# Kernel tuning notes

Measured on AMD Instinct MI355X. Metric: run time of the kernel, lower is better.

## Reference

```python
import jax, jax.numpy as jnp
import numpy as np

N = 50000      # nodes
E = 200000     # directed edges (before self loops)
F_IN = 78      # atom feature dim
H = 4          # heads
G = 512        # graphs in batch
HID = 1024
OUT = 128
NEG_SLOPE = 0.2


def gat_conv(x, edge_index, W, att_src, att_dst, bias, num_nodes):
    """PyG GATConv (concat=True, add_self_loops=True), eval mode (no dropout)."""
    heads, ch = att_src.shape
    h = (x @ W).reshape(num_nodes, heads, ch)          # [N,H,C]
    # add self loops
    loop = jnp.arange(num_nodes, dtype=edge_index.dtype)
    row = jnp.concatenate([edge_index[0], loop])        # source j
    col = jnp.concatenate([edge_index[1], loop])        # target i
    a_src = jnp.einsum('nhc,hc->nh', h, att_src)        # [N,H]
    a_dst = jnp.einsum('nhc,hc->nh', h, att_dst)
    e = jax.nn.leaky_relu(a_src[row] + a_dst[col], NEG_SLOPE)   # [Etot,H]
    # segment softmax over incoming edges of each target node
    m = jax.ops.segment_max(e, col, num_segments=num_nodes)
    e = jnp.exp(e - m[col])
    denom = jax.ops.segment_sum(e, col, num_segments=num_nodes)
    alpha = e / (denom[col] + 1e-16)                    # [Etot,H]
    msg = h[row] * alpha[:, :, None]                    # [Etot,H,C]
    out = jax.ops.segment_sum(msg, col, num_segments=num_nodes)
    return out.reshape(num_nodes, heads * ch) + bias


def setup_inputs() -> dict:
    key = jax.random.key(0)
    ks = jax.random.split(key, 20)
    def glorot(k, shape):
        fan = shape[0] + shape[-1]
        return jax.random.normal(k, shape, jnp.float32) * np.sqrt(2.0 / fan)
    x = jax.random.normal(ks[0], (N, F_IN), jnp.float32)
    edge_index = jax.random.randint(ks[1], (2, E), 0, N, jnp.int64)
    batch = jnp.sort(jax.random.randint(ks[2], (N,), 0, G, jnp.int64))
    d1 = F_IN
    d2 = F_IN * H
    d3 = F_IN * H * H
    return {
        'x': x, 'edge_index': edge_index, 'batch': batch,
        'W1': glorot(ks[3], (d1, H * d1)), 'as1': glorot(ks[4], (H, d1)),
        'ad1': glorot(ks[5], (H, d1)), 'b1': jnp.zeros((H * d1,), jnp.float32),
        'W2': glorot(ks[6], (d2, H * d2)), 'as2': glorot(ks[7], (H, d2)),
        'ad2': glorot(ks[8], (H, d2)), 'b2': jnp.zeros((H * d2,), jnp.float32),
        'W3': glorot(ks[9], (d3, d3)), 'as3': glorot(ks[10], (1, d3)),
        'ad3': glorot(ks[11], (1, d3)), 'b3': jnp.zeros((d3,), jnp.float32),
        'fc1_w': glorot(ks[12], (d3, HID)), 'fc1_b': jnp.zeros((HID,), jnp.float32),
        'fc2_w': glorot(ks[13], (HID, OUT)), 'fc2_b': jnp.zeros((OUT,), jnp.float32),
    }


def reference(x, edge_index, batch, W1, as1, ad1, b1, W2, as2, ad2, b2,
              W3, as3, ad3, b3, fc1_w, fc1_b, fc2_w, fc2_b):
    h = jax.nn.relu(gat_conv(x, edge_index, W1, as1, ad1, b1, N))
    h = jax.nn.relu(gat_conv(h, edge_index, W2, as2, ad2, b2, N))
    h = jax.nn.relu(gat_conv(h, edge_index, W3, as3, ad3, b3, N))
    g = jax.ops.segment_max(h, batch, num_segments=G)   # global max pool [G, 1248]
    g = jax.nn.relu(g @ fc1_w + fc1_b)
    # dropout is identity in eval mode
    out = jax.nn.relu(g @ fc2_w + fc2_b)
    return out
```

## Files before the change

kernel.cpp:

```cpp
#include <hip/hip_runtime.h>

using u16 = unsigned short;
using u32 = unsigned int;

typedef short s16x8 __attribute__((ext_vector_type(8)));
typedef float f32x4 __attribute__((ext_vector_type(4)));

static __device__ __forceinline__ float b2f(u16 u){ u32 x = ((u32)u) << 16; float f; __builtin_memcpy(&f, &x, 4); return f; }
static __device__ __forceinline__ u16 f2bf(float f){ u32 x; __builtin_memcpy(&x, &f, 4); x += 0x7fffu + ((x >> 16) & 1u); return (u16)(x >> 16); }

static __device__ __forceinline__ void async16(const u16* g, u16* l){
  __builtin_amdgcn_global_load_lds((const __attribute__((address_space(1))) u32*)g,
                                   (__attribute__((address_space(3))) u32*)l, 16, 0, 0);
}

__global__ void detect_flags(const u16* x, const int* ei, int* flags){
  if (blockIdx.x || threadIdx.x) return;
  int cf = 0;
  for (int i = 0; i < 128; ++i){
    int ex = (x[2*i] >> 7) & 0xff;
    if (ex >= 110 && ex <= 140) cf++;
  }
  flags[0] = (cf > 64) ? 1 : 0;
  int cz = 0;
  for (int i = 0; i < 128; ++i){ if (ei[2*i+1] != 0) cz++; }
  flags[1] = (cz > 64) ? 1 : 0;
}

__global__ void zero_u32(u32* p, int n){
  int i = blockIdx.x*256 + threadIdx.x;
  if (i < n) p[i] = 0;
}

__global__ void pad_copy_x(const void* xin, u16* xp, int Nreal, long tot, int F, int Fp, const int* flags){
  long idx = (long)blockIdx.x*256 + threadIdx.x;
  if (idx >= tot) return;
  int n = (int)(idx / Fp), f = (int)(idx - (long)n*Fp);
  u16 v = 0;
  if (n < Nreal && f < F){
    if (flags[0]) v = ((const u16*)xin)[(long)n*F + f];
    else          v = f2bf(((const float*)xin)[(long)n*F + f]);
  }
  xp[idx] = v;
}

__global__ void transpose_pad(const void* W, u16* Wt, int K, int Nsub, int Kp, int Np,
                              int ldW, int colOff, const int* flags){
  __shared__ u16 tile[32][33];
  int f0 = flags[0];
  int kb = blockIdx.x*32, nb = blockIdx.y*32;
  int tx = threadIdx.x & 31, ty = threadIdx.x >> 5;
  for (int dy = 0; dy < 32; dy += 8){
    int k = kb + dy + ty, n = nb + tx;
    u16 v = 0;
    if (k < K && n < Nsub){
      long src = (long)k*ldW + colOff + n;
      if (f0) v = ((const u16*)W)[src];
      else    v = f2bf(((const float*)W)[src]);
    }
    tile[dy+ty][tx] = v;
  }
  __syncthreads();
  for (int dy = 0; dy < 32; dy += 8){
    int n = nb + dy + ty, k = kb + tx;
    if (n < Np && k < Kp) Wt[(long)n*Kp + k] = tile[tx][dy+ty];
  }
}

__global__ void copy_vec5(const void* s0, u16* d0, int n0,
                          const void* s1, u16* d1, int n1,
                          const void* s2, u16* d2, int n2,
                          const void* s3, u16* d3, int n3,
                          const void* s4, u16* d4, int n4,
                          const int* flags){
  int i = blockIdx.x*256 + threadIdx.x;
  int f0 = flags[0];
  auto cv = [&](const void* s, int j)->u16{
    return f0 ? ((const u16*)s)[j] : f2bf(((const float*)s)[j]);
  };
  if (i < n0){ d0[i] = cv(s0, i); return; } i -= n0;
  if (i < n1){ d1[i] = cv(s1, i); return; } i -= n1;
  if (i < n2){ d2[i] = cv(s2, i); return; } i -= n2;
  if (i < n3){ d3[i] = cv(s3, i); return; } i -= n3;
  if (i < n4){ d4[i] = cv(s4, i); }
}

__global__ void copy_int3(const int* ei, const int* bat,
                          int* rowC, int* colC, int* bat32,
                          int E, int N, const int* flags){
  int i = blockIdx.x*256 + threadIdx.x;
  int f1 = flags[1];
  if (i < E){ rowC[i] = f1 ? ei[i] : ei[2*i]; return; } i -= E;
  if (i < E){ colC[i] = f1 ? ei[E + i] : ei[2*(E + i)]; return; } i -= E;
  if (i < N){ bat32[i] = f1 ? bat[i] : bat[2*i]; }
}

__global__ void hist_kernel(const int* __restrict__ colC, u32* cnt, int E){
  int e = blockIdx.x*256 + threadIdx.x;
  if (e < E) atomicAdd(&cnt[colC[e]], 1u);
}

__global__ void scan_local(const u32* __restrict__ cnt, u32* __restrict__ rowptr,
                           u32* __restrict__ bsum, int N){
  int blk = blockIdx.x, t = threadIdx.x;
  int i = blk*1024 + t;
  u32 v = (i < N) ? (cnt[i] + 1u) : 0u;
  u32 x = v;
  for (int off = 1; off < 64; off <<= 1){
    u32 y = __shfl_up(x, off);
    if ((t & 63) >= off) x += y;
  }
  __shared__ u32 ws[16];
  if ((t & 63) == 63) ws[t >> 6] = x;
  __syncthreads();
  if (t < 16){
    u32 y = ws[t];
    for (int off = 1; off < 16; off <<= 1){
      u32 z = __shfl_up(y, off);
      if (t >= off) y += z;
    }
    ws[t] = y;
  }
  __syncthreads();
  u32 base = (t >> 6) ? ws[(t >> 6) - 1] : 0u;
  u32 inc = base + x;
  if (i < N) rowptr[i + 1] = inc;
  if (t == 1023) bsum[blk] = inc;
}

__global__ void scan_bsums(const u32* __restrict__ bsum, u32* __restrict__ boff, int nb){
  int t = threadIdx.x;
  u32 v = (t < nb) ? bsum[t] : 0u;
  u32 x = v;
  for (int off = 1; off < 64; off <<= 1){
    u32 y = __shfl_up(x, off);
    if ((t & 63) >= off) x += y;
  }
  __shared__ u32 ws[16];
  if ((t & 63) == 63) ws[t >> 6] = x;
  __syncthreads();
  if (t < 16){
    u32 y = ws[t];
    for (int off = 1; off < 16; off <<= 1){
      u32 z = __shfl_up(y, off);
      if (t >= off) y += z;
    }
    ws[t] = y;
  }
  __syncthreads();
  u32 base = (t >> 6) ? ws[(t >> 6) - 1] : 0u;
  u32 inc = base + x;
  if (t < nb) boff[t] = inc - v;
}

__global__ void scan_fixup(u32* rowptr, const u32* __restrict__ boff, int N){
  int i = blockIdx.x*1024 + threadIdx.x;
  if (i < N) rowptr[i+1] += boff[blockIdx.x];
  if (i == 0) rowptr[0] = 0;
}

__global__ void fill_self(const u32* rowptr, int* eidx, u32* cursor, int N){
  int i = blockIdx.x*256 + threadIdx.x;
  if (i >= N) return;
  eidx[rowptr[i]] = i;
  cursor[i] = rowptr[i] + 1;
}

__global__ void fill_edges(const int* __restrict__ rowC, const int* __restrict__ colC,
                           u32* cursor, int* eidx, int E){
  int e = blockIdx.x*256 + threadIdx.x;
  if (e >= E) return;
  u32 pos = atomicAdd(&cursor[colC[e]], 1u);
  eidx[pos] = rowC[e];
}

__global__ void wproj(const void* W, const void* as, const void* ad,
                      float* wsrc, float* wdst, int Cin, int Cpad, int Chead, int ldW,
                      int H, const int* flags){
  int wid = blockIdx.x*4 + (threadIdx.x >> 6);
  if (wid >= H*Cpad) return;
  int h = wid / Cpad, c = wid - h*Cpad;
  int lane = threadIdx.x & 63;
  float s = 0.f, d = 0.f;
  if (c < Cin){
    int f0 = flags[0];
    long base = (long)c*ldW + (long)h*Chead;
    const long av0 = (long)h*Chead;
    for (int o = lane; o < Chead; o += 64){
      float wv = f0 ? b2f(((const u16*)W)[base+o]) : ((const float*)W)[base+o];
      float avv = f0 ? b2f(((const u16*)as)[av0+o]) : ((const float*)as)[av0+o];
      float dvv = f0 ? b2f(((const u16*)ad)[av0+o]) : ((const float*)ad)[av0+o];
      s += wv*avv; d += wv*dvv;
    }
    for (int off = 32; off; off >>= 1){ s += __shfl_down(s, off); d += __shfl_down(d, off); }
  }
  if (lane == 0){ wsrc[(long)h*Cpad+c] = s; wdst[(long)h*Cpad+c] = d; }
}

template<int H>
__global__ void attn_dots_v(const u16* __restrict__ xin, long ldx,
                            const float* __restrict__ wsrc, const float* __restrict__ wdst,
                            float* __restrict__ a_src, float* __restrict__ a_dst,
                            int Nn, int C){
  int node = blockIdx.x*4 + (threadIdx.x >> 6);
  if (node >= Nn) return;
  int lane = threadIdx.x & 63;
  const u16* xr = xin + (long)node*ldx;
  float s[H], d[H];
#pragma unroll
  for (int h = 0; h < H; ++h){ s[h] = 0.f; d[h] = 0.f; }
  for (int c = lane*8; c < C; c += 512){
    s16x8 xv = *(const s16x8*)&xr[c];
    float xf[8];
#pragma unroll
    for (int j = 0; j < 8; ++j) xf[j] = b2f((u16)xv[j]);
#pragma unroll
    for (int h = 0; h < H; ++h){
      f32x4 w0 = *(const f32x4*)&wsrc[h*C + c];
      f32x4 w1 = *(const f32x4*)&wsrc[h*C + c + 4];
      f32x4 d0 = *(const f32x4*)&wdst[h*C + c];
      f32x4 d1 = *(const f32x4*)&wdst[h*C + c + 4];
#pragma unroll
      for (int j = 0; j < 4; ++j){
        s[h] += xf[j]*w0[j] + xf[j+4]*w1[j];
        d[h] += xf[j]*d0[j] + xf[j+4]*d1[j];
      }
    }
  }
#pragma unroll
  for (int h = 0; h < H; ++h)
    for (int off = 32; off; off >>= 1){ s[h] += __shfl_down(s[h], off); d[h] += __shfl_down(d[h], off); }
  if (lane == 0){
#pragma unroll
    for (int h = 0; h < H; ++h){ a_src[(long)node*H+h] = s[h]; a_dst[(long)node*H+h] = d[h]; }
  }
}

__global__ void attn_stats(const u32* __restrict__ rowptr, const int* __restrict__ eidx,
                           const float* __restrict__ a_src, const float* __restrict__ a_dst,
                           u16* __restrict__ pbuf, float* __restrict__ invd, int NH, int H){
  int idx = blockIdx.x*256 + threadIdx.x;
  if (idx >= NH) return;
  int i = idx / H, hd = idx - i*H;
  u32 s0 = rowptr[i], s1 = rowptr[i+1];
  float ad = a_dst[idx];
  float m = -1e30f;
  for (u32 p = s0; p < s1; ++p){
    float e = a_src[eidx[p]*H + hd] + ad;
    e = e > 0.f ? e : 0.2f*e;
    m = fmaxf(m, e);
  }
  float den = 0.f;
  for (u32 p = s0; p < s1; ++p){
    float e = a_src[eidx[p]*H + hd] + ad;
    e = e > 0.f ? e : 0.2f*e;
    float v = __expf(e - m);
    pbuf[(long)p*H + hd] = f2bf(v);
    den += v;
  }
  invd[idx] = 1.f / (den + 1e-16f);
}

__global__ void aggregate_v(const u32* __restrict__ rowptr, const int* __restrict__ eidx,
                            const u16* __restrict__ pbuf, const float* __restrict__ invd,
                            const u16* __restrict__ xin, long ldx,
                            u16* __restrict__ xagg, long ldagg,
                            int chunks, int H, int headStride){
  int i = blockIdx.x;
  int t = threadIdx.x;
  if (t >= H*chunks) return;
  int h = t / chunks, ck = t - h*chunks;
  int c0 = ck*8;
  u32 s0 = rowptr[i], s1 = rowptr[i+1];
  float acc[8];
#pragma unroll
  for (int j = 0; j < 8; ++j) acc[j] = 0.f;
  u32 p = s0;
  for (; p + 2 <= s1; p += 2){
    int sa = eidx[p], sb = eidx[p+1];
    float wa = b2f(pbuf[(long)p*H + h]);
    float wb = b2f(pbuf[(long)(p+1)*H + h]);
    s16x8 va = *(const s16x8*)&xin[(long)sa*ldx + c0];
    s16x8 vb = *(const s16x8*)&xin[(long)sb*ldx + c0];
#pragma unroll
    for (int j = 0; j < 8; ++j) acc[j] += wa*b2f((u16)va[j]) + wb*b2f((u16)vb[j]);
  }
  if (p < s1){
    int sa = eidx[p];
    float wa = b2f(pbuf[(long)p*H + h]);
    s16x8 va = *(const s16x8*)&xin[(long)sa*ldx + c0];
#pragma unroll
    for (int j = 0; j < 8; ++j) acc[j] += wa*b2f((u16)va[j]);
  }
  float inv = invd[(long)i*H + h];
  s16x8 ov;
#pragma unroll
  for (int j = 0; j < 8; ++j) ov[j] = (short)f2bf(acc[j]*inv);
  *(s16x8*)&xagg[(long)i*ldagg + h*headStride + c0] = ov;
}

__global__ void pack_pool(const u32* __restrict__ poolf, u16* __restrict__ pooled, int n){
  int i = blockIdx.x*256 + threadIdx.x;
  if (i >= n) return;
  u32 b = poolf[i]; float f; __builtin_memcpy(&f, &b, 4);
  pooled[i] = f2bf(f);
}

template<int NH>
__global__ __launch_bounds__(256) void gemm_bt(
    const u16* __restrict__ Ag, long lda, const u16* __restrict__ Bg,
    const u16* __restrict__ bias, u16* __restrict__ Cg,
    int M, int Nstore, int K, long ldc, int mode, const int* flags,
    const int* __restrict__ batg, u32* poolf, long ldp,
    int nt, int mt, long hA, long hB, long hC)
{
  const int xcd = blockIdx.x & 7;
  const int g = blockIdx.x >> 3;
  const u16 *A, *B, *bi; u16* C;
  int ntile, m;
  if constexpr (NH > 1){
    const int nhnt = NH * nt;
    const int inner = g % nhnt;
    ntile = inner % nt;
    const int head = inner / nt;
    m = (g / nhnt)*8 + xcd;
    A = Ag + (long)head*hA; B = Bg + (long)head*hB;
    bi = bias + (long)head*hC; C = Cg + (long)head*hC;
  } else {
    ntile = g % nt;
    m = (g / nt)*8 + xcd;
    A = Ag; B = Bg; bi = bias; C = Cg;
  }
  if (m >= mt) return;

  __shared__ __align__(16) u16 As[128*32];
  __shared__ __align__(16) u16 Bs[128*32];
  const int tid = threadIdx.x;
  const int wave = tid >> 6, lane = tid & 63;
  const int quad = lane >> 4, mrow = lane & 15;
  const int wm = (wave >> 1) * 64, wn = (wave & 1) * 64;
  const long bm = (long)m * 128;
  const long bn = (long)ntile * 128;

  f32x4 acc[4][4];
#pragma unroll
  for (int i = 0; i < 4; i++)
#pragma unroll
    for (int j = 0; j < 4; j++) acc[i][j] = (f32x4){0.f, 0.f, 0.f, 0.f};

  const int r0 = wave*32 + (lane >> 2);
  const int r1 = r0 + 16;
  const int kcl = lane & 3;
  const int q0 = kcl ^ ((r0 >> 1) & 3);
  const int q1 = kcl ^ ((r1 >> 1) & 3);
  const u16* a0 = A + (bm + r0)*lda + q0*8;
  const u16* a1 = A + (bm + r1)*lda + q1*8;
  const u16* b0 = B + (bn + r0)*(long)K + q0*8;
  const u16* b1 = B + (bn + r1)*(long)K + q1*8;
  u16* la0 = &As[r0*32 + kcl*8];
  u16* la1 = &As[r1*32 + kcl*8];
  u16* lb0 = &Bs[r0*32 + kcl*8];
  u16* lb1 = &Bs[r1*32 + kcl*8];

  for (int k0 = 0; k0 < K; k0 += 32){
    async16(a0 + k0, la0);
    async16(a1 + k0, la1);
    async16(b0 + k0, lb0);
    async16(b1 + k0, lb1);
    __syncthreads();
    s16x8 af[4], bf[4];
#pragma unroll
    for (int i = 0; i < 4; i++){
      int r = wm + i*16 + mrow;
      int q = quad ^ ((r >> 1) & 3);
      af[i] = *(const s16x8*)&As[r*32 + q*8];
    }
#pragma unroll
    for (int j = 0; j < 4; j++){
      int r = wn + j*16 + mrow;
      int q = quad ^ ((r >> 1) & 3);
      bf[j] = *(const s16x8*)&Bs[r*32 + q*8];
    }
#pragma unroll
    for (int i = 0; i < 4; i++)
#pragma unroll
      for (int j = 0; j < 4; j++)
        acc[i][j] = __builtin_amdgcn_mfma_f32_16x16x32_bf16(af[i], bf[j], acc[i][j], 0, 0, 0);
    __syncthreads();
  }

  if (mode & 4){
    int garr[16];
#pragma unroll
    for (int i = 0; i < 4; i++)
#pragma unroll
      for (int r = 0; r < 4; r++){
        long row = bm + wm + i*16 + quad*4 + r;
        garr[i*4+r] = (row < M) ? batg[row] : -1;
      }
#pragma unroll
    for (int j = 0; j < 4; j++){
      long col = bn + wn + j*16 + mrow;
      if (col >= Nstore) continue;
      float bv = b2f(bi[col]);
      int curg = -1; float curm = 0.f;
#pragma unroll
      for (int i = 0; i < 4; i++)
#pragma unroll
        for (int r = 0; r < 4; r++){
          int g2 = garr[i*4+r];
          if (g2 >= 0){
            float v = fmaxf(acc[i][j][r] + bv, 0.f);
            if (g2 != curg){
              if (curg >= 0){
                u32 bits; __builtin_memcpy(&bits, &curm, 4);
                atomicMax(&poolf[(long)curg*ldp + col], bits);
              }
              curg = g2; curm = v;
            } else curm = fmaxf(curm, v);
          }
        }
      if (curg >= 0){
        u32 bits; __builtin_memcpy(&bits, &curm, 4);
        atomicMax(&poolf[(long)curg*ldp + col], bits);
      }
    }
    return;
  }

  const int f0 = (mode & 2) ? flags[0] : 1;
#pragma unroll
  for (int i = 0; i < 4; i++){
    long row0 = bm + wm + i*16 + quad*4;
#pragma unroll
    for (int j = 0; j < 4; j++){
      long col = bn + wn + j*16 + mrow;
      if (col < Nstore){
        float bv = (mode & 1) ? b2f(bi[col]) : 0.f;
#pragma unroll
        for (int r = 0; r < 4; r++){
          long row = row0 + r;
          if (row < M){
            float v = acc[i][j][r];
            if (mode & 1) v = fmaxf(v + bv, 0.f);
            if (f0) C[row*ldc + col] = f2bf(v);
            else    ((float*)C)[row*ldc + col] = v;
          }
        }
      }
    }
  }
}

extern "C" void kernel_launch(void* const* d_in, const int* in_sizes, int n_in,
                              void* d_out, int out_size, void* d_ws, size_t ws_size,
                              hipStream_t stream){
  const u16* x    = (const u16*)d_in[0];
  const int* ei   = (const int*)d_in[1];
  const int* bat  = (const int*)d_in[2];
  const void* W1  = d_in[3];
  const void* as1 = d_in[4]; const void* ad1 = d_in[5]; const void* b1 = d_in[6];
  const void* W2  = d_in[7];
  const void* as2 = d_in[8]; const void* ad2 = d_in[9]; const void* b2 = d_in[10];
  const void* W3  = d_in[11];
  const void* as3 = d_in[12]; const void* ad3 = d_in[13]; const void* b3 = d_in[14];
  const void* fc1w = d_in[15]; const void* fc1b = d_in[16];
  const void* fc2w = d_in[17]; const void* fc2b = d_in[18];

  const int E = in_sizes[1] / 2;
  const int N = in_sizes[2];
  const int G = 512, H = 4;
  const int Mpad = ((N + 127)/128)*128;
  const int Etot = E + N;
  const int Mt = Mpad/128;
  const int nb1024 = (N + 1023)/1024;
  const int Mg8 = ((Mt + 7)/8);

  char* w = (char*)d_ws;
  size_t off = 0;
  auto AL = [&](size_t b)->char*{ char* p = w + off; off = (off + b + 255) & ~(size_t)255; return p; };

  u16* P = (u16*)AL((size_t)Mpad*1248*2 + 512);
  u16* Q = (u16*)AL((size_t)Mpad*1248*2 + 512);
  u16* wt1 = (u16*)AL((size_t)4*128*96*2);
  u16* wt2 = (u16*)AL((size_t)4*384*320*2);
  u16* wt3 = (u16*)AL((size_t)1280*1248*2);
  u16* wf1 = (u16*)AL((size_t)1024*1248*2);
  u16* wf2 = (u16*)AL((size_t)128*1024*2);
  u16* cb1 = (u16*)AL(312*2);  u16* cb2 = (u16*)AL(1248*2); u16* cb3 = (u16*)AL(1248*2);
  u16* cbf1 = (u16*)AL(1024*2); u16* cbf2 = (u16*)AL(128*2);
  float* ws1 = (float*)AL(4*80*4);   float* wd1 = (float*)AL(4*80*4);
  float* ws2 = (float*)AL(4*312*4);  float* wd2 = (float*)AL(4*312*4);
  float* ws3 = (float*)AL(1248*4);   float* wd3 = (float*)AL(1248*4);
  float* a_src = (float*)AL((size_t)N*H*4);
  float* a_dst = (float*)AL((size_t)N*H*4);
  float* invd  = (float*)AL((size_t)N*H*4);
  u16*  pbuf   = (u16*)AL((size_t)Etot*H*2);
  u32* cnt     = (u32*)AL((size_t)N*4);
  u32* rowptr  = (u32*)AL((size_t)(N+1)*4);
  u32* bsum    = (u32*)AL((size_t)1024*4);
  u32* boff    = (u32*)AL((size_t)1024*4);
  int* eidx    = (int*)AL((size_t)Etot*4);
  int* bat32   = (int*)AL((size_t)N*4);
  u32* poolf   = (u32*)AL((size_t)G*1248*4);
  u16* pooled  = (u16*)AL((size_t)G*1248*2 + 512);
  u16* fc1o    = (u16*)AL((size_t)G*1024*2 + 512);
  int* flags   = (int*)AL(16);

  if (ws_size < off || n_in < 19) return;

  u16* xpad = (u16*)((char*)P + ((size_t)40 << 20));
  int* rowC = (int*)((char*)Q + ((size_t)64 << 20));
  int* colC = rowC + E;

  detect_flags<<<1, 64, 0, stream>>>(x, ei, flags);
  zero_u32<<<(N+255)/256, 256, 0, stream>>>(cnt, N);
  zero_u32<<<(G*1248+255)/256, 256, 0, stream>>>(poolf, G*1248);
  {
    long tot = (long)Mpad*96;
    pad_copy_x<<<(unsigned)((tot+255)/256), 256, 0, stream>>>(x, xpad, N, tot, 78, 96, flags);
  }
  for (int h = 0; h < 4; ++h)
    transpose_pad<<<dim3(3,4),  256, 0, stream>>>(W1, wt1 + h*128*96, 78, 78, 96, 128, 312, h*78, flags);
  for (int h = 0; h < 4; ++h)
    transpose_pad<<<dim3(10,12), 256, 0, stream>>>(W2, wt2 + h*384*320, 312, 312, 320, 384, 1248, h*312, flags);
  transpose_pad<<<dim3(39,40), 256, 0, stream>>>(W3,   wt3, 1248, 1248, 1248, 1280, 1248, 0, flags);
  transpose_pad<<<dim3(39,32), 256, 0, stream>>>(fc1w, wf1, 1248, 1024, 1248, 1024, 1024, 0, flags);
  transpose_pad<<<dim3(32,4),  256, 0, stream>>>(fc2w, wf2, 1024, 128,  1024, 128,  128,  0, flags);
  copy_vec5<<<(312+1248+1248+1024+128+255)/256, 256, 0, stream>>>(
      b1, cb1, 312, b2, cb2, 1248, b3, cb3, 1248, fc1b, cbf1, 1024, fc2b, cbf2, 128, flags);
  copy_int3<<<(E+E+N+255)/256, 256, 0, stream>>>(ei, bat, rowC, colC, bat32, E, N, flags);
  wproj<<<(4*80+3)/4,   256, 0, stream>>>(W1, as1, ad1, ws1, wd1, 78, 80, 78, 312, 4, flags);
  wproj<<<(4*312+3)/4,  256, 0, stream>>>(W2, as2, ad2, ws2, wd2, 312, 312, 312, 1248, 4, flags);
  wproj<<<(1248+3)/4,   256, 0, stream>>>(W3, as3, ad3, ws3, wd3, 1248, 1248, 1248, 1248, 1, flags);

  hist_kernel<<<(E+255)/256, 256, 0, stream>>>(colC, cnt, E);
  scan_local<<<nb1024, 1024, 0, stream>>>(cnt, rowptr, bsum, N);
  scan_bsums<<<1, 1024, 0, stream>>>(bsum, boff, nb1024);
  scan_fixup<<<nb1024, 1024, 0, stream>>>(rowptr, boff, N);
  fill_self<<<(N+255)/256, 256, 0, stream>>>(rowptr, eidx, cnt, N);
  fill_edges<<<(E+255)/256, 256, 0, stream>>>(rowC, colC, cnt, eidx, E);

  const int db = (N + 3)/4;

  attn_dots_v<4><<<db, 256, 0, stream>>>(xpad, 96, ws1, wd1, a_src, a_dst, N, 80);
  attn_stats<<<(N*4+255)/256, 256, 0, stream>>>(rowptr, eidx, a_src, a_dst, pbuf, invd, N*4, 4);
  aggregate_v<<<N, 64, 0, stream>>>(rowptr, eidx, pbuf, invd, xpad, 96, Q, 384, 10, 4, 96);
  gemm_bt<4><<<Mg8*4*1*8, 256, 0, stream>>>(Q, 384, wt1, cb1, P, N, 78, 96, 312, 1, flags,
                                            nullptr, nullptr, 0, 1, Mt, 96, 128*96, 78);

  attn_dots_v<4><<<db, 256, 0, stream>>>(P, 312, ws2, wd2, a_src, a_dst, N, 312);
  attn_stats<<<(N*4+255)/256, 256, 0, stream>>>(rowptr, eidx, a_src, a_dst, pbuf, invd, N*4, 4);
  aggregate_v<<<N, 192, 0, stream>>>(rowptr, eidx, pbuf, invd, P, 312, Q, 1248, 39, 4, 312);
  gemm_bt<4><<<Mg8*4*3*8, 256, 0, stream>>>(Q, 1248, wt2, cb2, P, N, 312, 320, 1248, 1, flags,
                                            nullptr, nullptr, 0, 3, Mt, 312, 384*320, 312);

  attn_dots_v<1><<<db, 256, 0, stream>>>(P, 1248, ws3, wd3, a_src, a_dst, N, 1248);
  attn_stats<<<(N+255)/256, 256, 0, stream>>>(rowptr, eidx, a_src, a_dst, pbuf, invd, N, 1);
  aggregate_v<<<N, 192, 0, stream>>>(rowptr, eidx, pbuf, invd, P, 1248, Q, 1248, 156, 1, 0);
  gemm_bt<1><<<Mg8*10*8, 256, 0, stream>>>(Q, 1248, wt3, cb3, P, N, 1248, 1248, 1248, 1|4, flags,
                                           bat32, poolf, 1248, 10, Mt, 0, 0, 0);

  pack_pool<<<(G*1248+255)/256, 256, 0, stream>>>(poolf, pooled, G*1248);
  gemm_bt<1><<<64, 256, 0, stream>>>(pooled, 1248, wf1, cbf1, fc1o, G, 1024, 1248, 1024, 1, flags,
                                     nullptr, nullptr, 0, 8, 4, 0, 0, 0);
  gemm_bt<1><<<8, 256, 0, stream>>>(fc1o, 1024, wf2, cbf2, (u16*)d_out, G, 128, 1024, 128, 3, flags,
                                    nullptr, nullptr, 0, 1, 4, 0, 0, 0);
}
```

Before: 1.064 ms.

## Fuse segment softmax stats into aggregation and batch setup kernel launches

Removes the separate attn_stats kernel and its bf16 probability buffer. Each aggregation block now computes an online max and denominator per head, then recomputes edge weights into shared memory in chunks before gathering neighbor features. It also merges the two zeroing launches into one contiguous zero (reordering allocations so poolf follows cnt), folds the per-head transpose launches into a z-grid dimension, and parallelizes flag detection across a wavefront. The cost is a serial per-node stats loop on a few threads plus extra syncs and exp recomputation inside each aggregation block.

```diff
diff --git a/kernel.cpp b/kernel.cpp
--- a/kernel.cpp
+++ b/kernel.cpp
@@ -15,20 +15,19 @@
 }
 
 __global__ void detect_flags(const u16* x, const int* ei, int* flags){
-  if (blockIdx.x || threadIdx.x) return;
-  int cf = 0;
-  for (int i = 0; i < 128; ++i){
+  int lane = threadIdx.x & 63;
+  int cf = 0, cz = 0;
+  for (int i = lane; i < 128; i += 64){
     int ex = (x[2*i] >> 7) & 0xff;
     if (ex >= 110 && ex <= 140) cf++;
-  }
-  flags[0] = (cf > 64) ? 1 : 0;
-  int cz = 0;
-  for (int i = 0; i < 128; ++i){ if (ei[2*i+1] != 0) cz++; }
-  flags[1] = (cz > 64) ? 1 : 0;
-}
-
-__global__ void zero_u32(u32* p, int n){
-  int i = blockIdx.x*256 + threadIdx.x;
+    if (ei[2*i+1] != 0) cz++;
+  }
+  for (int off = 32; off; off >>= 1){ cf += __shfl_down(cf, off); cz += __shfl_down(cz, off); }
+  if (lane == 0){ flags[0] = (cf > 64) ? 1 : 0; flags[1] = (cz > 64) ? 1 : 0; }
+}
+
+__global__ void zero_u32(u32* p, long n){
+  long i = (long)blockIdx.x*256 + threadIdx.x;
   if (i < n) p[i] = 0;
 }
 
@@ -45,9 +44,12 @@
 }
 
 __global__ void transpose_pad(const void* W, u16* Wt, int K, int Nsub, int Kp, int Np,
-                              int ldW, int colOff, const int* flags){
+                              int ldW, long wtStride, int colOffStep, const int* flags){
   __shared__ u16 tile[32][33];
   int f0 = flags[0];
+  int z = blockIdx.z;
+  u16* Wtz = Wt + (long)z*wtStride;
+  int colOff = z*colOffStep;
   int kb = blockIdx.x*32, nb = blockIdx.y*32;
   int tx = threadIdx.x & 31, ty = threadIdx.x >> 5;
   for (int dy = 0; dy < 32; dy += 8){
@@ -63,7 +65,7 @@
   __syncthreads();
   for (int dy = 0; dy < 32; dy += 8){
     int n = nb + dy + ty, k = kb + tx;
-    if (n < Np && k < Kp) Wt[(long)n*Kp + k] = tile[tx][dy+ty];
+    if (n < Np && k < Kp) Wtz[(long)n*Kp + k] = tile[tx][dy+ty];
   }
 }
 
@@ -236,67 +238,76 @@
   }
 }
 
-__global__ void attn_stats(const u32* __restrict__ rowptr, const int* __restrict__ eidx,
-                           const float* __restrict__ a_src, const float* __restrict__ a_dst,
-                           u16* __restrict__ pbuf, float* __restrict__ invd, int NH, int H){
-  int idx = blockIdx.x*256 + threadIdx.x;
-  if (idx >= NH) return;
-  int i = idx / H, hd = idx - i*H;
-  u32 s0 = rowptr[i], s1 = rowptr[i+1];
-  float ad = a_dst[idx];
-  float m = -1e30f;
-  for (u32 p = s0; p < s1; ++p){
-    float e = a_src[eidx[p]*H + hd] + ad;
-    e = e > 0.f ? e : 0.2f*e;
-    m = fmaxf(m, e);
-  }
-  float den = 0.f;
-  for (u32 p = s0; p < s1; ++p){
-    float e = a_src[eidx[p]*H + hd] + ad;
-    e = e > 0.f ? e : 0.2f*e;
-    float v = __expf(e - m);
-    pbuf[(long)p*H + hd] = f2bf(v);
-    den += v;
-  }
-  invd[idx] = 1.f / (den + 1e-16f);
-}
-
-__global__ void aggregate_v(const u32* __restrict__ rowptr, const int* __restrict__ eidx,
-                            const u16* __restrict__ pbuf, const float* __restrict__ invd,
-                            const u16* __restrict__ xin, long ldx,
-                            u16* __restrict__ xagg, long ldagg,
-                            int chunks, int H, int headStride){
+template<int H>
+__global__ void agg_fused(const u32* __restrict__ rowptr, const int* __restrict__ eidx,
+                          const float* __restrict__ a_src, const float* __restrict__ a_dst,
+                          const u16* __restrict__ xin, long ldx,
+                          u16* __restrict__ xagg, long ldagg,
+                          int chunks, int headStride){
+  constexpr int CH = 256;
+  __shared__ int ssrc[CH];
+  __shared__ float sw[CH*H];
+  __shared__ float sm[H], sden[H], sad[H];
   int i = blockIdx.x;
   int t = threadIdx.x;
-  if (t >= H*chunks) return;
+  int bd = blockDim.x;
+  u32 s0 = rowptr[i], s1 = rowptr[i+1];
+  if (t < H){
+    float ad = a_dst[(long)i*H + t];
+    sad[t] = ad;
+    float m = -1e30f, den = 0.f;
+    for (u32 p = s0; p < s1; ++p){
+      float e = a_src[(long)eidx[p]*H + t] + ad;
+      e = e > 0.f ? e : 0.2f*e;
+      if (e > m){ den *= __expf(m - e); m = e; }
+      den += __expf(e - m);
+    }
+    sm[t] = m; sden[t] = 1.f/(den + 1e-16f);
+  }
   int h = t / chunks, ck = t - h*chunks;
   int c0 = ck*8;
-  u32 s0 = rowptr[i], s1 = rowptr[i+1];
+  bool active = (t < H*chunks);
   float acc[8];
 #pragma unroll
   for (int j = 0; j < 8; ++j) acc[j] = 0.f;
-  u32 p = s0;
-  for (; p + 2 <= s1; p += 2){
-    int sa = eidx[p], sb = eidx[p+1];
-    float wa = b2f(pbuf[(long)p*H + h]);
-    float wb = b2f(pbuf[(long)(p+1)*H + h]);
-    s16x8 va = *(const s16x8*)&xin[(long)sa*ldx + c0];
-    s16x8 vb = *(const s16x8*)&xin[(long)sb*ldx + c0];
-#pragma unroll
-    for (int j = 0; j < 8; ++j) acc[j] += wa*b2f((u16)va[j]) + wb*b2f((u16)vb[j]);
-  }
-  if (p < s1){
-    int sa = eidx[p];
-    float wa = b2f(pbuf[(long)p*H + h]);
-    s16x8 va = *(const s16x8*)&xin[(long)sa*ldx + c0];
-#pragma unroll
-    for (int j = 0; j < 8; ++j) acc[j] += wa*b2f((u16)va[j]);
-  }
-  float inv = invd[(long)i*H + h];
-  s16x8 ov;
-#pragma unroll
-  for (int j = 0; j < 8; ++j) ov[j] = (short)f2bf(acc[j]*inv);
-  *(s16x8*)&xagg[(long)i*ldagg + h*headStride + c0] = ov;
+  for (u32 base = s0; base < s1; base += CH){
+    int cnt = (int)((s1 - base < (u32)CH) ? (s1 - base) : (u32)CH);
+    __syncthreads();
+    for (int j = t; j < cnt; j += bd){
+      int src = eidx[base + j];
+      ssrc[j] = src;
+#pragma unroll
+      for (int hh = 0; hh < H; ++hh){
+        float e = a_src[(long)src*H + hh] + sad[hh];
+        e = e > 0.f ? e : 0.2f*e;
+        sw[j*H + hh] = __expf(e - sm[hh]);
+      }
+    }
+    __syncthreads();
+    if (active){
+      int j = 0;
+      for (; j + 2 <= cnt; j += 2){
+        float wa = sw[j*H + h], wb = sw[(j+1)*H + h];
+        s16x8 va = *(const s16x8*)&xin[(long)ssrc[j]*ldx + c0];
+        s16x8 vb = *(const s16x8*)&xin[(long)ssrc[j+1]*ldx + c0];
+#pragma unroll
+        for (int q = 0; q < 8; ++q) acc[q] += wa*b2f((u16)va[q]) + wb*b2f((u16)vb[q]);
+      }
+      if (j < cnt){
+        float wa = sw[j*H + h];
+        s16x8 va = *(const s16x8*)&xin[(long)ssrc[j]*ldx + c0];
+#pragma unroll
+        for (int q = 0; q < 8; ++q) acc[q] += wa*b2f((u16)va[q]);
+      }
+    }
+  }
+  if (active){
+    float inv = sden[h];
+    s16x8 ov;
+#pragma unroll
+    for (int q = 0; q < 8; ++q) ov[q] = (short)f2bf(acc[q]*inv);
+    *(s16x8*)&xagg[(long)i*ldagg + h*headStride + c0] = ov;
+  }
 }
 
 __global__ void pack_pool(const u32* __restrict__ poolf, u16* __restrict__ pooled, int n){
@@ -494,15 +505,13 @@
   float* ws3 = (float*)AL(1248*4);   float* wd3 = (float*)AL(1248*4);
   float* a_src = (float*)AL((size_t)N*H*4);
   float* a_dst = (float*)AL((size_t)N*H*4);
-  float* invd  = (float*)AL((size_t)N*H*4);
-  u16*  pbuf   = (u16*)AL((size_t)Etot*H*2);
   u32* cnt     = (u32*)AL((size_t)N*4);
+  u32* poolf   = (u32*)AL((size_t)G*1248*4);
   u32* rowptr  = (u32*)AL((size_t)(N+1)*4);
   u32* bsum    = (u32*)AL((size_t)1024*4);
   u32* boff    = (u32*)AL((size_t)1024*4);
   int* eidx    = (int*)AL((size_t)Etot*4);
   int* bat32   = (int*)AL((size_t)N*4);
-  u32* poolf   = (u32*)AL((size_t)G*1248*4);
   u16* pooled  = (u16*)AL((size_t)G*1248*2 + 512);
   u16* fc1o    = (u16*)AL((size_t)G*1024*2 + 512);
   int* flags   = (int*)AL(16);
@@ -514,19 +523,19 @@
   int* colC = rowC + E;
 
   detect_flags<<<1, 64, 0, stream>>>(x, ei, flags);
-  zero_u32<<<(N+255)/256, 256, 0, stream>>>(cnt, N);
-  zero_u32<<<(G*1248+255)/256, 256, 0, stream>>>(poolf, G*1248);
+  {
+    long zlen = (long)(poolf - cnt) + (long)G*1248;
+    zero_u32<<<(unsigned)((zlen+255)/256), 256, 0, stream>>>(cnt, zlen);
+  }
   {
     long tot = (long)Mpad*96;
     pad_copy_x<<<(unsigned)((tot+255)/256), 256, 0, stream>>>(x, xpad, N, tot, 78, 96, flags);
   }
-  for (int h = 0; h < 4; ++h)
-    transpose_pad<<<dim3(3,4),  256, 0, stream>>>(W1, wt1 + h*128*96, 78, 78, 96, 128, 312, h*78, flags);
-  for (int h = 0; h < 4; ++h)
-    transpose_pad<<<dim3(10,12), 256, 0, stream>>>(W2, wt2 + h*384*320, 312, 312, 320, 384, 1248, h*312, flags);
-  transpose_pad<<<dim3(39,40), 256, 0, stream>>>(W3,   wt3, 1248, 1248, 1248, 1280, 1248, 0, flags);
-  transpose_pad<<<dim3(39,32), 256, 0, stream>>>(fc1w, wf1, 1248, 1024, 1248, 1024, 1024, 0, flags);
-  transpose_pad<<<dim3(32,4),  256, 0, stream>>>(fc2w, wf2, 1024, 128,  1024, 128,  128,  0, flags);
+  transpose_pad<<<dim3(3,4,4),   256, 0, stream>>>(W1,   wt1, 78,   78,   96,   128,  312,  128*96,  78,  flags);
+  transpose_pad<<<dim3(10,12,4), 256, 0, stream>>>(W2,   wt2, 312,  312,  320,  384,  1248, 384*320, 312, flags);
+  transpose_pad<<<dim3(39,40,1), 256, 0, stream>>>(W3,   wt3, 1248, 1248, 1248, 1280, 1248, 0, 0, flags);
+  transpose_pad<<<dim3(39,32,1), 256, 0, stream>>>(fc1w, wf1, 1248, 1024, 1248, 1024, 1024, 0, 0, flags);
+  transpose_pad<<<dim3(32,4,1),  256, 0, stream>>>(fc2w, wf2, 1024, 128,  1024, 128,  128,  0, 0, flags);
   copy_vec5<<<(312+1248+1248+1024+128+255)/256, 256, 0, stream>>>(
       b1, cb1, 312, b2, cb2, 1248, b3, cb3, 1248, fc1b, cbf1, 1024, fc2b, cbf2, 128, flags);
   copy_int3<<<(E+E+N+255)/256, 256, 0, stream>>>(ei, bat, rowC, colC, bat32, E, N, flags);
@@ -544,20 +553,17 @@
   const int db = (N + 3)/4;
 
   attn_dots_v<4><<<db, 256, 0, stream>>>(xpad, 96, ws1, wd1, a_src, a_dst, N, 80);
-  attn_stats<<<(N*4+255)/256, 256, 0, stream>>>(rowptr, eidx, a_src, a_dst, pbuf, invd, N*4, 4);
-  aggregate_v<<<N, 64, 0, stream>>>(rowptr, eidx, pbuf, invd, xpad, 96, Q, 384, 10, 4, 96);
+  agg_fused<4><<<N, 64, 0, stream>>>(rowptr, eidx, a_src, a_dst, xpad, 96, Q, 384, 10, 96);
   gemm_bt<4><<<Mg8*4*1*8, 256, 0, stream>>>(Q, 384, wt1, cb1, P, N, 78, 96, 312, 1, flags,
                                             nullptr, nullptr, 0, 1, Mt, 96, 128*96, 78);
 
   attn_dots_v<4><<<db, 256, 0, stream>>>(P, 312, ws2, wd2, a_src, a_dst, N, 312);
-  attn_stats<<<(N*4+255)/256, 256, 0, stream>>>(rowptr, eidx, a_src, a_dst, pbuf, invd, N*4, 4);
-  aggregate_v<<<N, 192, 0, stream>>>(rowptr, eidx, pbuf, invd, P, 312, Q, 1248, 39, 4, 312);
+  agg_fused<4><<<N, 192, 0, stream>>>(rowptr, eidx, a_src, a_dst, P, 312, Q, 1248, 39, 312);
   gemm_bt<4><<<Mg8*4*3*8, 256, 0, stream>>>(Q, 1248, wt2, cb2, P, N, 312, 320, 1248, 1, flags,
                                             nullptr, nullptr, 0, 3, Mt, 312, 384*320, 312);
 
   attn_dots_v<1><<<db, 256, 0, stream>>>(P, 1248, ws3, wd3, a_src, a_dst, N, 1248);
-  attn_stats<<<(N+255)/256, 256, 0, stream>>>(rowptr, eidx, a_src, a_dst, pbuf, invd, N, 1);
-  aggregate_v<<<N, 192, 0, stream>>>(rowptr, eidx, pbuf, invd, P, 1248, Q, 1248, 156, 1, 0);
+  agg_fused<1><<<N, 192, 0, stream>>>(rowptr, eidx, a_src, a_dst, P, 1248, Q, 1248, 156, 0);
   gemm_bt<1><<<Mg8*10*8, 256, 0, stream>>>(Q, 1248, wt3, cb3, P, N, 1248, 1248, 1248, 1|4, flags,
                                            bat32, poolf, 1248, 10, Mt, 0, 0, 0);
 
```

Measured after the change: 1.082 ms. About the same (+1.7%).
